# Performance work log

Measured on AMD Instinct MI355X. Metric: run time of the kernel, lower is better.

The kernel has to match this reference:

```python
import jax, jax.numpy as jnp
import numpy as np

NEG_INF = -1000000.0
B_, NG, HEADS, C, GH, GW, GD = 256, 64, 6, 192, 6, 6, 6
N = GH * GW * GD
POS_DIM = (C // 4) // 4  # DynamicPosBias(dim//4): pos_dim = (dim//4)//4 = 12


def setup_inputs() -> dict:
    key = jax.random.key(0)
    ks = jax.random.split(key, 12)
    rn = lambda k, shape, s=0.02: jax.random.normal(k, shape, jnp.float32) * s
    x = jax.random.normal(ks[0], (B_, N, C), jnp.float32)
    y = jax.random.normal(ks[1], (B_, N, C), jnp.float32)
    # 0 / -1e6 window mask, as produced by the padding logic upstream
    mask = jnp.where(jax.random.bernoulli(ks[2], 0.1, (NG, N, N)), NEG_INF, 0.0).astype(jnp.float32)
    return dict(
        x=x, y=y, mask=mask,
        Wqkv=rn(ks[3], (3 * C, C)), bqkv=jnp.zeros((3 * C,), jnp.float32),
        Wproj=rn(ks[4], (C, C)), bproj=jnp.zeros((C,), jnp.float32),
        pos_proj_w=rn(ks[5], (POS_DIM, 3)), pos_proj_b=jnp.zeros((POS_DIM,), jnp.float32),
        ln1_g=jnp.ones((POS_DIM,), jnp.float32), ln1_b=jnp.zeros((POS_DIM,), jnp.float32),
        pos1_w=rn(ks[6], (POS_DIM, POS_DIM)), pos1_b=jnp.zeros((POS_DIM,), jnp.float32),
        ln2_g=jnp.ones((POS_DIM,), jnp.float32), ln2_b=jnp.zeros((POS_DIM,), jnp.float32),
        pos2_w=rn(ks[7], (POS_DIM, POS_DIM)), pos2_b=jnp.zeros((POS_DIM,), jnp.float32),
        ln3_g=jnp.ones((POS_DIM,), jnp.float32), ln3_b=jnp.zeros((POS_DIM,), jnp.float32),
        pos3_w=rn(ks[8], (HEADS, POS_DIM)), pos3_b=jnp.zeros((HEADS,), jnp.float32),
        H=GH, W=GW, D=GD)


def _ln(t, g, b):
    m = t.mean(-1, keepdims=True)
    v = ((t - m) ** 2).mean(-1, keepdims=True)
    return (t - m) / jnp.sqrt(v + 1e-5) * g + b


def _rel_tables(H, W, D):
    # biases: all relative offsets in [1-H,H-1]x[1-W,W-1]x[1-D,D-1], shape (M, 3)
    ph = np.arange(1 - H, H); pw = np.arange(1 - W, W); pd = np.arange(1 - D, D)
    biases = np.stack(np.meshgrid(ph, pw, pd, indexing='ij')).reshape(3, -1).T.astype(np.float32)
    coords = np.stack(np.meshgrid(np.arange(H), np.arange(W), np.arange(D), indexing='ij')).reshape(3, -1)
    rel = (coords[:, :, None] - coords[:, None, :]).transpose(1, 2, 0)  # (N, N, 3)
    rel[..., 0] += H - 1; rel[..., 1] += W - 1; rel[..., 2] += D - 1
    rel[..., 0] *= (2 * W - 1) * (2 * D - 1); rel[..., 1] *= (2 * D - 1)
    idx = rel.sum(-1)  # (N, N) indices into the (M,) bias table
    return jnp.asarray(biases), jnp.asarray(idx)


def reference(x, y, mask, Wqkv, bqkv, Wproj, bproj, pos_proj_w, pos_proj_b,
              ln1_g, ln1_b, pos1_w, pos1_b, ln2_g, ln2_b, pos2_w, pos2_b,
              ln3_g, ln3_b, pos3_w, pos3_b, H, W, D):
    Bt, n, c = x.shape
    heads = pos3_w.shape[0]
    hd = c // heads
    scale = hd ** (-0.5)
    # NOTE: original code applies self.qkv to BOTH x and y (qkv_y layer unused)
    qkv = (x @ Wqkv.T + bqkv).reshape(Bt, n, 3, heads, hd).transpose(2, 0, 3, 1, 4)
    qkv_y = (y @ Wqkv.T + bqkv).reshape(Bt, n, 3, heads, hd).transpose(2, 0, 3, 1, 4)
    q = qkv[0] * scale
    k_y, v_y = qkv_y[1], qkv_y[2]
    attn = jnp.einsum('bhnd,bhmd->bhnm', q, k_y)
    # dynamic relative position bias: tiny MLP over offsets, then gather
    biases, idx = _rel_tables(H, W, D)
    pos = biases @ pos_proj_w.T + pos_proj_b
    pos = jnp.maximum(_ln(pos, ln1_g, ln1_b), 0) @ pos1_w.T + pos1_b
    pos = jnp.maximum(_ln(pos, ln2_g, ln2_b), 0) @ pos2_w.T + pos2_b
    pos = jnp.maximum(_ln(pos, ln3_g, ln3_b), 0) @ pos3_w.T + pos3_b  # (M, heads)
    rpb = pos[idx.reshape(-1)].reshape(n, n, heads).transpose(2, 0, 1)  # (heads, N, N)
    attn = attn + rpb[None]
    nG = mask.shape[0]
    attn = attn.reshape(Bt // nG, nG, heads, n, n) + mask[None, :, None]
    attn = jax.nn.softmax(attn, axis=-1).reshape(Bt, heads, n, n)
    out = jnp.einsum('bhnm,bhmd->bhnd', attn, v_y).transpose(0, 2, 1, 3).reshape(Bt, n, c)
    return out @ Wproj.T + bproj
```

## Files before the change

kernel.cpp:

```cpp
#include <hip/hip_runtime.h>
#include <stdint.h>

using short8   = __attribute__((ext_vector_type(8))) short;
using float4_  = __attribute__((ext_vector_type(4))) float;
using ushort4_ = __attribute__((ext_vector_type(4))) unsigned short;
typedef unsigned int  uint;
typedef unsigned short ushort;

__device__ __forceinline__ float bf2f(ushort b) {
  uint u = ((uint)b) << 16;
  return __builtin_bit_cast(float, u);
}
__device__ __forceinline__ ushort f2bf(float f) {
  uint u = __builtin_bit_cast(uint, f);
  u = u + 0x7fffu + ((u >> 16) & 1u);
  return (ushort)(u >> 16);
}

#define NN   216
#define NSQ  46656
#define PADV (-3.0e6f)

#define WA_WQKV   0
#define WA_BQKV   110592
#define WA_WPROJ  111168
#define WA_BPROJ  148032
#define WA_PPW    148224
#define WA_PPB    148260
#define WA_G1     148272
#define WA_B1     148284
#define WA_W1     148296
#define WA_WB1    148440
#define WA_G2     148452
#define WA_B2     148464
#define WA_W2     148476
#define WA_WB2    148620
#define WA_G3     148632
#define WA_B3     148644
#define WA_W3     148656
#define WA_WB3    148728
#define WA_TOTAL  148740

__global__ void detect_kernel(const uint* __restrict__ x, int* __restrict__ flag) {
  int lane = threadIdx.x;
  uint w = x[lane];
  ushort lo = (ushort)(w & 0xffffu);
  int e = (lo >> 7) & 0xff;
  int sane = (lo == 0 || (e >= 0x60 && e <= 0x9f)) ? 1 : 0;
  unsigned long long b = __ballot(sane);
  if (lane == 0) flag[0] = (__popcll(b) >= 56) ? 0 : 1;
}

struct SrcPtrs { const void* p[18]; };

__global__ void convert_kernel(SrcPtrs sp, ushort* __restrict__ dst,
                               const int* __restrict__ flag) {
  constexpr int OFF[19] = {WA_WQKV, WA_BQKV, WA_WPROJ, WA_BPROJ, WA_PPW, WA_PPB,
                           WA_G1, WA_B1, WA_W1, WA_WB1, WA_G2, WA_B2, WA_W2,
                           WA_WB2, WA_G3, WA_B3, WA_W3, WA_WB3, WA_TOTAL};
  int t = blockIdx.x * 256 + threadIdx.x;
  if (t >= WA_TOTAL) return;
  int a = 0;
#pragma unroll
  for (int i = 1; i < 18; ++i) a += (t >= OFF[i]) ? 1 : 0;
  int local = t - OFF[a];
  const void* s = sp.p[a];
  ushort v;
  if (flag[0]) v = f2bf(((const float*)s)[local]);
  else         v = ((const ushort*)s)[local];
  dst[t] = v;
}

__device__ __forceinline__ void ln_relu(const float* p, const ushort* g,
                                        const ushort* b, float* r) {
  float m = 0.f;
#pragma unroll
  for (int t = 0; t < 12; ++t) m += p[t];
  m *= (1.f / 12.f);
  float v = 0.f;
#pragma unroll
  for (int t = 0; t < 12; ++t) { float d = p[t] - m; v += d * d; }
  v *= (1.f / 12.f);
  float inv = rsqrtf(v + 1e-5f);
#pragma unroll
  for (int t = 0; t < 12; ++t) {
    float z = (p[t] - m) * inv * bf2f(g[t]) + bf2f(b[t]);
    r[t] = fmaxf(z, 0.f);
  }
}

__global__ void pos_mlp_kernel(const ushort* __restrict__ wa, float* __restrict__ pos) {
  int m = blockIdx.x * blockDim.x + threadIdx.x;
  if (m >= 1331) return;
  const ushort* pw  = wa + WA_PPW;  const ushort* pb  = wa + WA_PPB;
  const ushort* g1  = wa + WA_G1;   const ushort* b1  = wa + WA_B1;
  const ushort* w1  = wa + WA_W1;   const ushort* wb1 = wa + WA_WB1;
  const ushort* g2  = wa + WA_G2;   const ushort* b2  = wa + WA_B2;
  const ushort* w2  = wa + WA_W2;   const ushort* wb2 = wa + WA_WB2;
  const ushort* g3  = wa + WA_G3;   const ushort* b3  = wa + WA_B3;
  const ushort* w3  = wa + WA_W3;   const ushort* wb3 = wa + WA_WB3;

  int ih = m / 121, rem = m - ih * 121;
  int iw = rem / 11, id = rem - iw * 11;
  float fh = (float)(ih - 5), fw = (float)(iw - 5), fd = (float)(id - 5);
  float p[12], r[12], q[12];
#pragma unroll
  for (int t = 0; t < 12; ++t)
    p[t] = fh * bf2f(pw[t * 3]) + fw * bf2f(pw[t * 3 + 1]) +
           fd * bf2f(pw[t * 3 + 2]) + bf2f(pb[t]);
  ln_relu(p, g1, b1, r);
#pragma unroll
  for (int t = 0; t < 12; ++t) {
    float s = bf2f(wb1[t]);
#pragma unroll
    for (int u = 0; u < 12; ++u) s += r[u] * bf2f(w1[t * 12 + u]);
    q[t] = s;
  }
  ln_relu(q, g2, b2, r);
#pragma unroll
  for (int t = 0; t < 12; ++t) {
    float s = bf2f(wb2[t]);
#pragma unroll
    for (int u = 0; u < 12; ++u) s += r[u] * bf2f(w2[t * 12 + u]);
    p[t] = s;
  }
  ln_relu(p, g3, b3, r);
#pragma unroll
  for (int h = 0; h < 6; ++h) {
    float s = bf2f(wb3[h]);
#pragma unroll
    for (int u = 0; u < 12; ++u) s += r[u] * bf2f(w3[h * 12 + u]);
    pos[m * 6 + h] = s;
  }
}

__global__ void rpbfrag_kernel(const float* __restrict__ pos, ushort* __restrict__ out) {
  int tgl = blockIdx.x * 256 + threadIdx.x;
  if (tgl >= 6 * 196 * 64) return;
  int lane = tgl & 63;
  int tj   = (tgl >> 6) % 196;
  int h    = (tgl >> 6) / 196;
  int tt = tj / 14, j = tj - tt * 14;
  int l16 = lane & 15, quad = lane >> 4;
  int col = j * 16 + l16;
  int h2 = col / 36, r2 = col - h2 * 36, w2 = r2 / 6, d2 = r2 - w2 * 6;
  ushort4_ o;
#pragma unroll
  for (int r = 0; r < 4; ++r) {
    int i = tt * 16 + quad * 4 + r;
    float val = PADV;
    if (i < 216 && col < 216) {
      int h1 = i / 36, r1 = i - h1 * 36, w1 = r1 / 6, d1 = r1 - w1 * 6;
      int idx = ((h1 - h2 + 5) * 11 + (w1 - w2 + 5)) * 11 + (d1 - d2 + 5);
      val = pos[idx * 6 + h];
    }
    o[r] = f2bf(val);
  }
  *(ushort4_*)(out + (size_t)tgl * 4) = o;
}

__global__ void maskfrag_kernel(const void* __restrict__ maskv,
                                const int* __restrict__ flag,
                                ushort* __restrict__ out) {
  int tgl = blockIdx.x * 256 + threadIdx.x;
  if (tgl >= 64 * 196 * 64) return;
  bool mf32 = flag[0] != 0;
  int lane = tgl & 63;
  int tj   = (tgl >> 6) % 196;
  int g    = (tgl >> 6) / 196;
  int tt = tj / 14, j = tj - tt * 14;
  int l16 = lane & 15, quad = lane >> 4;
  int col = j * 16 + l16;
  const float*  mf = (const float*)maskv + (size_t)g * NSQ;
  const ushort* mu = (const ushort*)maskv + (size_t)g * NSQ;
  ushort4_ o;
#pragma unroll
  for (int r = 0; r < 4; ++r) {
    int i = tt * 16 + quad * 4 + r;
    float val = PADV;
    if (i < 216 && col < 216) {
      int mi = i * 216 + col;
      val = mf32 ? mf[mi] : bf2f(mu[mi]);
    }
    o[r] = f2bf(val);
  }
  *(ushort4_*)(out + (size_t)tgl * 4) = o;
}

__global__ __launch_bounds__(256) void gemm_kernel(
    const void* __restrict__ Ax, const void* __restrict__ Ay,
    const ushort* __restrict__ W,  const ushort* __restrict__ bias,
    void* __restrict__ dq, void* __restrict__ dk, void* __restrict__ dv,
    const int* __restrict__ flag, int is_proj) {
  __shared__ __align__(16) ushort a_lds[128 * 72];
  __shared__ __align__(16) ushort b_lds[192 * 72];
  int tid = threadIdx.x;
  int m0 = blockIdx.x * 128;
  int z  = blockIdx.z;
  const void* A = (z == 0) ? Ax : Ay;
  int wbase = is_proj ? 0 : z * 192;
  float scale = (!is_proj && z == 0) ? 0.17677669529663687f : 1.0f;
  void* dst = (z == 0) ? dq : (z == 1 ? dk : dv);
  bool a_f32 = (!is_proj) && (flag[0] != 0);
  bool o_f32 = is_proj && (flag[0] != 0);

  int lane = tid & 63, w = tid >> 6;
  int l16 = lane & 15, quad = lane >> 4;
  int wm = w >> 1, wn = w & 1;

  float4_ acc[4][6];
#pragma unroll
  for (int mt = 0; mt < 4; ++mt)
#pragma unroll
    for (int nt = 0; nt < 6; ++nt) acc[mt][nt] = (float4_){0.f, 0.f, 0.f, 0.f};

  for (int kc = 0; kc < 3; ++kc) {
    for (int i = tid; i < 1024; i += 256) {
      int row = i >> 3, c8 = i & 7;
      short8 pk;
      if (a_f32) {
        const float* Af = (const float*)A + (size_t)(m0 + row) * 192 + kc * 64 + c8 * 8;
        float4_ lo = *(const float4_*)Af;
        float4_ hi = *(const float4_*)(Af + 4);
#pragma unroll
        for (int jj = 0; jj < 4; ++jj) {
          pk[jj]     = (short)f2bf(lo[jj]);
          pk[4 + jj] = (short)f2bf(hi[jj]);
        }
      } else {
        pk = *(const short8*)((const ushort*)A + (size_t)(m0 + row) * 192 + kc * 64 + c8 * 8);
      }
      *(short8*)(a_lds + row * 72 + c8 * 8) = pk;
    }
    for (int i = tid; i < 1536; i += 256) {
      int row = i >> 3, c8 = i & 7;
      short8 pk = *(const short8*)(W + (size_t)(wbase + row) * 192 + kc * 64 + c8 * 8);
      *(short8*)(b_lds + row * 72 + c8 * 8) = pk;
    }
    __syncthreads();
#pragma unroll
    for (int kk = 0; kk < 2; ++kk) {
      short8 af[4], bfr[6];
#pragma unroll
      for (int mt = 0; mt < 4; ++mt)
        af[mt] = *(const short8*)(a_lds + (wm * 64 + mt * 16 + l16) * 72 + kk * 32 + quad * 8);
#pragma unroll
      for (int nt = 0; nt < 6; ++nt)
        bfr[nt] = *(const short8*)(b_lds + (wn * 96 + nt * 16 + l16) * 72 + kk * 32 + quad * 8);
#pragma unroll
      for (int mt = 0; mt < 4; ++mt)
#pragma unroll
        for (int nt = 0; nt < 6; ++nt)
          acc[mt][nt] = __builtin_amdgcn_mfma_f32_16x16x32_bf16(af[mt], bfr[nt], acc[mt][nt], 0, 0, 0);
    }
    __syncthreads();
  }

#pragma unroll
  for (int mt = 0; mt < 4; ++mt) {
#pragma unroll
    for (int nt = 0; nt < 6; ++nt) {
      int lcol = wn * 96 + nt * 16 + l16;
      float bv = bf2f(bias[(is_proj ? 0 : z * 192) + lcol]);
#pragma unroll
      for (int r = 0; r < 4; ++r) {
        int grow = m0 + wm * 64 + mt * 16 + quad * 4 + r;
        float val = (acc[mt][nt][r] + bv) * scale;
        if (is_proj) {
          if (o_f32) ((float*)dst)[(size_t)grow * 192 + lcol] = val;
          else       ((ushort*)dst)[(size_t)grow * 192 + lcol] = f2bf(val);
        } else {
          int bb = grow / 216;
          int nn2 = grow - bb * 216;
          int hh = lcol >> 5, dd = lcol & 31;
          ((ushort*)dst)[(((size_t)bb * 6 + hh) * 216 + nn2) * 32 + dd] = f2bf(val);
        }
      }
    }
  }
}

__global__ __launch_bounds__(256) void attn_kernel(
    const ushort* __restrict__ q, const ushort* __restrict__ k,
    const ushort* __restrict__ v, const ushort* __restrict__ rpbf,
    const ushort* __restrict__ maskf, ushort* __restrict__ opre) {
  __shared__ __align__(16) ushort vts[32 * 232];
  __shared__ __align__(16) ushort ps[4][16 * 232];

  int bid = blockIdx.x;
  int b = bid / 6, h = bid - b * 6;
  int g = b & 63;
  int tid = threadIdx.x, lane = tid & 63, w = tid >> 6;
  int l16 = lane & 15, quad = lane >> 4;

  const ushort* qh = q + (size_t)(b * 6 + h) * 6912;
  const ushort* kh = k + (size_t)(b * 6 + h) * 6912;
  const ushort* vh = v + (size_t)(b * 6 + h) * 6912;

  for (int i = tid; i < (32 * 232) / 2; i += 256) ((uint*)vts)[i] = 0u;
  __syncthreads();
  for (int i = tid; i < 864; i += 256) {
    int n = i >> 2, dp = (i & 3) * 8;
    uint4 raw = *(const uint4*)(vh + n * 32 + dp);
    const ushort* ep = reinterpret_cast<const ushort*>(&raw);
#pragma unroll
    for (int jj = 0; jj < 8; ++jj) vts[(dp + jj) * 232 + n] = ep[jj];
  }
  __syncthreads();

  for (int t = w; t < 14; t += 4) {
    int r0 = t * 16;
    const ushort* rf = rpbf  + ((size_t)(h * 196 + t * 14) * 64 + lane) * 4;
    const ushort* mf = maskf + ((size_t)(g * 196 + t * 14) * 64 + lane) * 4;
    short8 aq = *(const short8*)(qh + (r0 + l16) * 32 + quad * 8);

    float4_ s[14];
#pragma unroll
    for (int j = 0; j < 14; ++j) {
      ushort4_ rb = *(const ushort4_*)(rf + j * 256);
      ushort4_ mb = *(const ushort4_*)(mf + j * 256);
      float4_ cin;
#pragma unroll
      for (int r = 0; r < 4; ++r) cin[r] = bf2f(rb[r]) + bf2f(mb[r]);
      short8 bk = *(const short8*)(kh + (j * 16 + l16) * 32 + quad * 8);
      s[j] = __builtin_amdgcn_mfma_f32_16x16x32_bf16(aq, bk, cin, 0, 0, 0);
    }

#pragma unroll
    for (int r = 0; r < 4; ++r) {
      float mx = -1e30f;
#pragma unroll
      for (int j = 0; j < 14; ++j) mx = fmaxf(mx, s[j][r]);
      mx = fmaxf(mx, __shfl_xor(mx, 1));
      mx = fmaxf(mx, __shfl_xor(mx, 2));
      mx = fmaxf(mx, __shfl_xor(mx, 4));
      mx = fmaxf(mx, __shfl_xor(mx, 8));
      float sum = 0.f;
#pragma unroll
      for (int j = 0; j < 14; ++j) {
        float pe = __expf(s[j][r] - mx);
        s[j][r] = pe;
        sum += pe;
      }
      sum += __shfl_xor(sum, 1);
      sum += __shfl_xor(sum, 2);
      sum += __shfl_xor(sum, 4);
      sum += __shfl_xor(sum, 8);
      float inv = 1.0f / sum;
#pragma unroll
      for (int j = 0; j < 14; ++j)
        ps[w][(quad * 4 + r) * 232 + j * 16 + l16] = f2bf(s[j][r] * inv);
    }

    asm volatile("s_waitcnt lgkmcnt(0)" ::: "memory");

    float4_ o0 = (float4_){0.f, 0.f, 0.f, 0.f};
    float4_ o1 = (float4_){0.f, 0.f, 0.f, 0.f};
#pragma unroll
    for (int kt = 0; kt < 7; ++kt) {
      short8 pf = *(const short8*)(&ps[w][l16 * 232 + kt * 32 + quad * 8]);
      short8 v0 = *(const short8*)(&vts[(l16) * 232 + kt * 32 + quad * 8]);
      short8 v1 = *(const short8*)(&vts[(16 + l16) * 232 + kt * 32 + quad * 8]);
      o0 = __builtin_amdgcn_mfma_f32_16x16x32_bf16(pf, v0, o0, 0, 0, 0);
      o1 = __builtin_amdgcn_mfma_f32_16x16x32_bf16(pf, v1, o1, 0, 0, 0);
    }

#pragma unroll
    for (int r = 0; r < 4; ++r) {
      int i = r0 + quad * 4 + r;
      if (i < 216) {
        size_t base = ((size_t)b * 216 + i) * 192 + h * 32;
        opre[base + l16]      = f2bf(o0[r]);
        opre[base + 16 + l16] = f2bf(o1[r]);
      }
    }
  }
}

extern "C" void kernel_launch(void* const* d_in, const int* in_sizes, int n_in,
                              void* d_out, int out_size, void* d_ws, size_t ws_size,
                              hipStream_t stream) {
  (void)in_sizes; (void)n_in; (void)out_size; (void)ws_size;

  char* p = (char*)d_ws;
  int*    flag   = (int*)p;            p += 256;
  ushort* warena = (ushort*)p;         p += 298496 - 256;
  float*  pos    = (float*)p;          p += 32000;
  ushort* rpbf   = (ushort*)p;         p += 602112;
  ushort* maskf  = (ushort*)p;         p += 6422528;
  ushort* qb     = (ushort*)p;         p += 21234688;
  ushort* kb     = (ushort*)p;         p += 21234688;
  ushort* vb     = (ushort*)p;         p += 21234688;
  ushort* opre   = (ushort*)p;

  detect_kernel<<<1, 64, 0, stream>>>((const uint*)d_in[0], flag);

  SrcPtrs sp;
  for (int i = 0; i < 18; ++i) sp.p[i] = d_in[3 + i];
  convert_kernel<<<(WA_TOTAL + 255) / 256, 256, 0, stream>>>(sp, warena, flag);

  pos_mlp_kernel<<<6, 256, 0, stream>>>(warena, pos);
  rpbfrag_kernel<<<294, 256, 0, stream>>>(pos, rpbf);
  maskfrag_kernel<<<3136, 256, 0, stream>>>(d_in[2], flag, maskf);

  gemm_kernel<<<dim3(432, 1, 3), 256, 0, stream>>>(
      d_in[0], d_in[1], warena + WA_WQKV, warena + WA_BQKV,
      qb, kb, vb, flag, 0);

  attn_kernel<<<1536, 256, 0, stream>>>(qb, kb, vb, rpbf, maskf, opre);

  gemm_kernel<<<dim3(432, 1, 1), 256, 0, stream>>>(
      opre, opre, warena + WA_WPROJ, warena + WA_BPROJ,
      d_out, d_out, d_out, flag, 1);
}
```

Measured before the change: 336.4 us.

## Restructure QKV/proj GEMM: weights in LDS fragment layout, A streamed from global, y pre-converted

The GEMM now splits N across blockIdx.y, so each block covers 96 output columns. It loads the whole K=192 weight slice into LDS once, pre-arranged in MFMA fragment order, and reads A fragments straight from global memory into registers, which removes the per-k-chunk LDS staging and barriers. A separate cvt_kernel converts the fp32 y input to bf16 once, so the K and V passes read bf16 instead of each converting fp32 on the fly. In exchange, every A row is now read from global memory twice (once per N half), one more kernel launch is added, and a 21 MB buffer is reused for both ycvt and opre.

Measured after the change: 322.0 us. -4.3%, faster.

```diff
diff --git a/kernel.cpp b/kernel.cpp
--- a/kernel.cpp
+++ b/kernel.cpp
@@ -71,6 +71,22 @@
   dst[t] = v;
 }
 
+__global__ __launch_bounds__(256) void cvt_kernel(const float* __restrict__ src,
+                                                  ushort* __restrict__ dst,
+                                                  const int* __restrict__ flag) {
+  if (flag[0] == 0) return;
+  size_t s = ((size_t)blockIdx.x * 256 + threadIdx.x) * 8;
+  float4_ lo = *(const float4_*)(src + s);
+  float4_ hi = *(const float4_*)(src + s + 4);
+  short8 pk;
+#pragma unroll
+  for (int j = 0; j < 4; ++j) {
+    pk[j]     = (short)f2bf(lo[j]);
+    pk[4 + j] = (short)f2bf(hi[j]);
+  }
+  *(short8*)(dst + s) = pk;
+}
+
 __device__ __forceinline__ void ln_relu(const float* p, const ushort* g,
                                         const ushort* b, float* r) {
   float m = 0.f;
@@ -188,83 +204,89 @@
 }
 
 __global__ __launch_bounds__(256) void gemm_kernel(
-    const void* __restrict__ Ax, const void* __restrict__ Ay,
+    const void* __restrict__ p0,
+    const ushort* __restrict__ p1,
+    const void* __restrict__ p2,
     const ushort* __restrict__ W,  const ushort* __restrict__ bias,
     void* __restrict__ dq, void* __restrict__ dk, void* __restrict__ dv,
     const int* __restrict__ flag, int is_proj) {
-  __shared__ __align__(16) ushort a_lds[128 * 72];
-  __shared__ __align__(16) ushort b_lds[192 * 72];
+  __shared__ __align__(16) ushort b_lds[2304 * 8];
+
   int tid = threadIdx.x;
   int m0 = blockIdx.x * 128;
+  int n0 = blockIdx.y * 96;
   int z  = blockIdx.z;
-  const void* A = (z == 0) ? Ax : Ay;
   int wbase = is_proj ? 0 : z * 192;
   float scale = (!is_proj && z == 0) ? 0.17677669529663687f : 1.0f;
   void* dst = (z == 0) ? dq : (z == 1 ? dk : dv);
-  bool a_f32 = (!is_proj) && (flag[0] != 0);
-  bool o_f32 = is_proj && (flag[0] != 0);
+  int fl = flag[0];
+  bool f32path = (!is_proj) && (z == 0) && (fl != 0);
+  bool o_f32 = is_proj && (fl != 0);
+
+  const ushort* A16;
+  if (is_proj)      A16 = p1;
+  else if (z == 0)  A16 = (const ushort*)p0;
+  else              A16 = fl ? p1 : (const ushort*)p2;
+  const float* A32 = (const float*)p0;
 
   int lane = tid & 63, w = tid >> 6;
   int l16 = lane & 15, quad = lane >> 4;
-  int wm = w >> 1, wn = w & 1;
-
-  float4_ acc[4][6];
-#pragma unroll
-  for (int mt = 0; mt < 4; ++mt)
+
+  for (int s = tid; s < 2304; s += 256) {
+    int kk = s / 384;
+    int rem = s - kk * 384;
+    int nt = rem >> 6;
+    int l  = rem & 63;
+    int l16v = l & 15, qv = l >> 4;
+    short8 pk = *(const short8*)(W + (size_t)(wbase + n0 + nt * 16 + l16v) * 192 + kk * 32 + qv * 8);
+    *(short8*)(b_lds + s * 8) = pk;
+  }
+  __syncthreads();
+
+  float4_ acc[2][6];
+#pragma unroll
+  for (int mt = 0; mt < 2; ++mt)
 #pragma unroll
     for (int nt = 0; nt < 6; ++nt) acc[mt][nt] = (float4_){0.f, 0.f, 0.f, 0.f};
 
-  for (int kc = 0; kc < 3; ++kc) {
-    for (int i = tid; i < 1024; i += 256) {
-      int row = i >> 3, c8 = i & 7;
-      short8 pk;
-      if (a_f32) {
-        const float* Af = (const float*)A + (size_t)(m0 + row) * 192 + kc * 64 + c8 * 8;
-        float4_ lo = *(const float4_*)Af;
-        float4_ hi = *(const float4_*)(Af + 4);
-#pragma unroll
-        for (int jj = 0; jj < 4; ++jj) {
-          pk[jj]     = (short)f2bf(lo[jj]);
-          pk[4 + jj] = (short)f2bf(hi[jj]);
+#pragma unroll
+  for (int kk = 0; kk < 6; ++kk) {
+    short8 af[2];
+#pragma unroll
+    for (int mt = 0; mt < 2; ++mt) {
+      size_t abase = (size_t)(m0 + w * 32 + mt * 16 + l16) * 192 + kk * 32 + quad * 8;
+      if (f32path) {
+        float4_ lo = *(const float4_*)(A32 + abase);
+        float4_ hi = *(const float4_*)(A32 + abase + 4);
+#pragma unroll
+        for (int j = 0; j < 4; ++j) {
+          af[mt][j]     = (short)f2bf(lo[j]);
+          af[mt][4 + j] = (short)f2bf(hi[j]);
         }
       } else {
-        pk = *(const short8*)((const ushort*)A + (size_t)(m0 + row) * 192 + kc * 64 + c8 * 8);
+        af[mt] = *(const short8*)(A16 + abase);
       }
-      *(short8*)(a_lds + row * 72 + c8 * 8) = pk;
-    }
-    for (int i = tid; i < 1536; i += 256) {
-      int row = i >> 3, c8 = i & 7;
-      short8 pk = *(const short8*)(W + (size_t)(wbase + row) * 192 + kc * 64 + c8 * 8);
-      *(short8*)(b_lds + row * 72 + c8 * 8) = pk;
-    }
-    __syncthreads();
-#pragma unroll
-    for (int kk = 0; kk < 2; ++kk) {
-      short8 af[4], bfr[6];
-#pragma unroll
-      for (int mt = 0; mt < 4; ++mt)
-        af[mt] = *(const short8*)(a_lds + (wm * 64 + mt * 16 + l16) * 72 + kk * 32 + quad * 8);
+    }
+    short8 bfr[6];
+#pragma unroll
+    for (int nt = 0; nt < 6; ++nt)
+      bfr[nt] = *(const short8*)(b_lds + ((kk * 6 + nt) * 64 + lane) * 8);
+#pragma unroll
+    for (int mt = 0; mt < 2; ++mt)
 #pragma unroll
       for (int nt = 0; nt < 6; ++nt)
-        bfr[nt] = *(const short8*)(b_lds + (wn * 96 + nt * 16 + l16) * 72 + kk * 32 + quad * 8);
-#pragma unroll
-      for (int mt = 0; mt < 4; ++mt)
-#pragma unroll
-        for (int nt = 0; nt < 6; ++nt)
-          acc[mt][nt] = __builtin_amdgcn_mfma_f32_16x16x32_bf16(af[mt], bfr[nt], acc[mt][nt], 0, 0, 0);
-    }
-    __syncthreads();
-  }
-
-#pragma unroll
-  for (int mt = 0; mt < 4; ++mt) {
+        acc[mt][nt] = __builtin_amdgcn_mfma_f32_16x16x32_bf16(af[mt], bfr[nt], acc[mt][nt], 0, 0, 0);
+  }
+
+#pragma unroll
+  for (int mt = 0; mt < 2; ++mt) {
 #pragma unroll
     for (int nt = 0; nt < 6; ++nt) {
-      int lcol = wn * 96 + nt * 16 + l16;
+      int lcol = n0 + nt * 16 + l16;
       float bv = bf2f(bias[(is_proj ? 0 : z * 192) + lcol]);
 #pragma unroll
       for (int r = 0; r < 4; ++r) {
-        int grow = m0 + wm * 64 + mt * 16 + quad * 4 + r;
+        int grow = m0 + w * 32 + mt * 16 + quad * 4 + r;
         float val = (acc[mt][nt][r] + bv) * scale;
         if (is_proj) {
           if (o_f32) ((float*)dst)[(size_t)grow * 192 + lcol] = val;
@@ -384,14 +406,15 @@
 
   char* p = (char*)d_ws;
   int*    flag   = (int*)p;            p += 256;
-  ushort* warena = (ushort*)p;         p += 298496 - 256;
-  float*  pos    = (float*)p;          p += 32000;
+  ushort* warena = (ushort*)p;         p += 298240;
+  float*  pos    = (float*)p;          p += 32768;
   ushort* rpbf   = (ushort*)p;         p += 602112;
   ushort* maskf  = (ushort*)p;         p += 6422528;
+  ushort* ycvt   = (ushort*)p;         p += 21234688;
   ushort* qb     = (ushort*)p;         p += 21234688;
   ushort* kb     = (ushort*)p;         p += 21234688;
-  ushort* vb     = (ushort*)p;         p += 21234688;
-  ushort* opre   = (ushort*)p;
+  ushort* vb     = (ushort*)p;
+  ushort* opre   = ycvt;
 
   detect_kernel<<<1, 64, 0, stream>>>((const uint*)d_in[0], flag);
 
@@ -399,17 +422,19 @@
   for (int i = 0; i < 18; ++i) sp.p[i] = d_in[3 + i];
   convert_kernel<<<(WA_TOTAL + 255) / 256, 256, 0, stream>>>(sp, warena, flag);
 
+  cvt_kernel<<<5184, 256, 0, stream>>>((const float*)d_in[1], ycvt, flag);
+
   pos_mlp_kernel<<<6, 256, 0, stream>>>(warena, pos);
   rpbfrag_kernel<<<294, 256, 0, stream>>>(pos, rpbf);
   maskfrag_kernel<<<3136, 256, 0, stream>>>(d_in[2], flag, maskf);
 
-  gemm_kernel<<<dim3(432, 1, 3), 256, 0, stream>>>(
-      d_in[0], d_in[1], warena + WA_WQKV, warena + WA_BQKV,
+  gemm_kernel<<<dim3(432, 2, 3), 256, 0, stream>>>(
+      d_in[0], ycvt, d_in[1], warena + WA_WQKV, warena + WA_BQKV,
       qb, kb, vb, flag, 0);
 
   attn_kernel<<<1536, 256, 0, stream>>>(qb, kb, vb, rpbf, maskf, opre);
 
-  gemm_kernel<<<dim3(432, 1, 1), 256, 0, stream>>>(
-      opre, opre, warena + WA_WPROJ, warena + WA_BPROJ,
+  gemm_kernel<<<dim3(432, 2, 1), 256, 0, stream>>>(
+      opre, opre, opre, warena + WA_WPROJ, warena + WA_BPROJ,
       d_out, d_out, d_out, flag, 1);
 }
```
